# Kernel tuning notes

Hardware: AMD Instinct MI355X
Metric: run time of the kernel (lower is better)

The kernel has to match this reference:

```python
import jax, jax.numpy as jnp
import numpy as np

B, N, D = 4, 4096, 512
K = 16384          # codebook size
NUM_Q = 2          # residual quantizers (shared codebook)


def setup_inputs() -> dict:
    key = jax.random.key(0)
    ks = jax.random.split(key, 6)
    s = 1.0 / np.sqrt(D)
    return {
        "x": jax.random.normal(ks[0], (B, N, D), dtype=jnp.float32),
        "enc_w": jax.random.normal(ks[1], (D, D), dtype=jnp.float32) * s,
        "enc_b": jnp.zeros((D,), dtype=jnp.float32),
        "codebook": jax.random.normal(ks[2], (K, D), dtype=jnp.float32),
        "dec_w": jax.random.normal(ks[3], (D, D), dtype=jnp.float32) * s,
        "dec_b": jnp.zeros((D,), dtype=jnp.float32),
    }


def _residual_vq(z, codebook):
    # z: [B, N, D] -> flatten tokens
    flat = z.reshape(-1, z.shape[-1])          # [T, D]
    c_sq = jnp.sum(codebook * codebook, axis=-1)  # [K]
    q_sum = jnp.zeros_like(flat)
    residual = flat
    for _ in range(NUM_Q):
        # argmin of ||r - c||^2 == argmin of (||c||^2 - 2 r.c); skip ||r||^2
        dists = c_sq[None, :] - 2.0 * (residual @ codebook.T)  # [T, K]
        idx = jnp.argmin(dists, axis=-1)                       # [T]
        q = codebook[idx]                                      # gather [T, D]
        q_sum = q_sum + q
        residual = residual - q
    return q_sum.reshape(z.shape)


def reference(x, enc_w, enc_b, codebook, dec_w, dec_b):
    z = x @ enc_w.T + enc_b                     # encoder Linear(512 -> 512)
    q = _residual_vq(z, codebook)               # sum of per-stage code vectors
    z_tilde = z + jax.lax.stop_gradient(q - z)  # straight-through estimator
    x_recon = z_tilde @ dec_w.T + dec_b         # decoder Linear(512 -> 512)
    return x_recon
```

## Files before the change

### kernel.cpp

```cpp
#include <hip/hip_runtime.h>
#include <stdint.h>

constexpr int TT = 16384;
constexpr int DD = 512;
constexpr int KK = 16384;
constexpr int TOPK = 8;

typedef __bf16 bf16x8 __attribute__((ext_vector_type(8)));
typedef __bf16 bf16x4 __attribute__((ext_vector_type(4)));
typedef float f32x4 __attribute__((ext_vector_type(4)));

typedef const __attribute__((address_space(1))) void* gas_ptr;
typedef __attribute__((address_space(3))) void* las_ptr;

__device__ __forceinline__ unsigned long long pack_di(float d, int idx) {
    uint32_t u = __float_as_uint(d);
    u = (u & 0x80000000u) ? ~u : (u | 0x80000000u);
    return ((unsigned long long)u << 32) | (uint32_t)idx;
}

__device__ __forceinline__ unsigned long long umin64(unsigned long long a,
                                                     unsigned long long b) {
    return a < b ? a : b;
}

template<int MODE>
__global__ __launch_bounds__(256)
void gemm_mfma(const float* __restrict__ A, const float* __restrict__ A2,
               const float* __restrict__ W, const float* __restrict__ bias,
               float* __restrict__ out0, float* __restrict__ out1,
               __bf16* __restrict__ out2)
{
    __shared__ __bf16 Ah[128 * 64], Al[128 * 64];
    __shared__ __bf16 Bh[128 * 64], Bl[128 * 64];
    const int tid = threadIdx.x;
    const int lane = tid & 63;
    const int w = tid >> 6;
    const int row0 = blockIdx.y * 128;
    const int col0 = blockIdx.x * 128;

    f32x4 acc[2][8] = {};

    const int sr = tid >> 4;
    const int scol = (tid & 15) * 4;
    const int lcol = (((scol >> 3) ^ (sr & 7)) << 3) + (scol & 7);

    int a_off[2], b_off[8];
    #pragma unroll
    for (int mi = 0; mi < 2; ++mi) {
        const int ar = w * 32 + mi * 16 + (lane & 15);
        a_off[mi] = ar * 64 + (((lane >> 4) ^ (lane & 7)) << 3);
    }
    #pragma unroll
    for (int ni = 0; ni < 8; ++ni) {
        const int br = ni * 16 + (lane & 15);
        b_off[ni] = br * 64 + (((lane >> 4) ^ (lane & 7)) << 3);
    }

    for (int kb = 0; kb < 512; kb += 64) {
        __syncthreads();
        #pragma unroll
        for (int i = 0; i < 8; ++i) {
            const int r = i * 16 + sr;
            float4 v = *(const float4*)(A + (size_t)(row0 + r) * 512 + kb + scol);
            if (MODE == 1) {
                const float4 u = *(const float4*)(A2 + (size_t)(row0 + r) * 512 + kb + scol);
                v.x -= u.x; v.y -= u.y; v.z -= u.z; v.w -= u.w;
            }
            bf16x4 hv, lv;
            hv[0] = (__bf16)v.x; hv[1] = (__bf16)v.y; hv[2] = (__bf16)v.z; hv[3] = (__bf16)v.w;
            lv[0] = (__bf16)(v.x - (float)hv[0]); lv[1] = (__bf16)(v.y - (float)hv[1]);
            lv[2] = (__bf16)(v.z - (float)hv[2]); lv[3] = (__bf16)(v.w - (float)hv[3]);
            *(bf16x4*)(Ah + r * 64 + lcol) = hv;
            *(bf16x4*)(Al + r * 64 + lcol) = lv;

            const float4 x = *(const float4*)(W + (size_t)(col0 + r) * 512 + kb + scol);
            bf16x4 hw, lw;
            hw[0] = (__bf16)x.x; hw[1] = (__bf16)x.y; hw[2] = (__bf16)x.z; hw[3] = (__bf16)x.w;
            lw[0] = (__bf16)(x.x - (float)hw[0]); lw[1] = (__bf16)(x.y - (float)hw[1]);
            lw[2] = (__bf16)(x.z - (float)hw[2]); lw[3] = (__bf16)(x.w - (float)hw[3]);
            *(bf16x4*)(Bh + r * 64 + lcol) = hw;
            *(bf16x4*)(Bl + r * 64 + lcol) = lw;
        }
        __syncthreads();
        #pragma unroll
        for (int s = 0; s < 2; ++s) {
            const int sx = s * 32;
            bf16x8 ah[2], al[2];
            #pragma unroll
            for (int mi = 0; mi < 2; ++mi) {
                ah[mi] = *(const bf16x8*)(Ah + (a_off[mi] ^ sx));
                al[mi] = *(const bf16x8*)(Al + (a_off[mi] ^ sx));
            }
            #pragma unroll
            for (int ni = 0; ni < 8; ++ni) {
                const bf16x8 bh = *(const bf16x8*)(Bh + (b_off[ni] ^ sx));
                const bf16x8 bl = *(const bf16x8*)(Bl + (b_off[ni] ^ sx));
                #pragma unroll
                for (int mi = 0; mi < 2; ++mi) {
                    acc[mi][ni] = __builtin_amdgcn_mfma_f32_16x16x32_bf16(ah[mi], bh, acc[mi][ni], 0, 0, 0);
                    acc[mi][ni] = __builtin_amdgcn_mfma_f32_16x16x32_bf16(ah[mi], bl, acc[mi][ni], 0, 0, 0);
                    acc[mi][ni] = __builtin_amdgcn_mfma_f32_16x16x32_bf16(al[mi], bh, acc[mi][ni], 0, 0, 0);
                }
            }
        }
    }

    #pragma unroll
    for (int mi = 0; mi < 2; ++mi) {
        #pragma unroll
        for (int reg = 0; reg < 4; ++reg) {
            const int row = row0 + w * 32 + mi * 16 + (lane >> 4) * 4 + reg;
            #pragma unroll
            for (int ni = 0; ni < 8; ++ni) {
                const int col = col0 + ni * 16 + (lane & 15);
                const float o = acc[mi][ni][reg] + bias[col];
                out0[(size_t)row * 512 + col] = o;
                if (MODE == 0) {
                    out1[(size_t)row * 512 + col] = o;
                    out2[(size_t)row * 512 + col] = (__bf16)o;
                }
            }
        }
    }
}

__global__ __launch_bounds__(256)
void dist_approx(const __bf16* __restrict__ Rh,
                 const __bf16* __restrict__ Ch,
                 const float* __restrict__ csq,
                 unsigned long long* __restrict__ winners)
{
    __shared__ __bf16 As[128 * 64];
    __shared__ __bf16 Bs[128 * 64];
    const int tid = threadIdx.x;
    const int lane = tid & 63;
    const int w = tid >> 6;
    const int row0 = blockIdx.y * 128;
    const int col0 = blockIdx.x * 128;

    f32x4 acc[2][8] = {};

    const int gc = (lane & 7) ^ ((lane >> 3) & 7);
    const __bf16* Ab = Rh + (size_t)(row0 + w * 32 + (lane >> 3)) * 512 + gc * 8;
    const __bf16* Bb = Ch + (size_t)(col0 + w * 32 + (lane >> 3)) * 512 + gc * 8;
    __bf16* lA = As + (w * 32) * 64;
    __bf16* lB = Bs + (w * 32) * 64;

    int a_off[2], b_off[8];
    #pragma unroll
    for (int mi = 0; mi < 2; ++mi) {
        const int ar = w * 32 + mi * 16 + (lane & 15);
        a_off[mi] = ar * 64 + (((lane >> 4) ^ (lane & 7)) << 3);
    }
    #pragma unroll
    for (int ni = 0; ni < 8; ++ni) {
        const int br = ni * 16 + (lane & 15);
        b_off[ni] = br * 64 + (((lane >> 4) ^ (lane & 7)) << 3);
    }

    for (int kb = 0; kb < 512; kb += 64) {
        __syncthreads();
        #pragma unroll
        for (int j = 0; j < 4; ++j) {
            __builtin_amdgcn_global_load_lds(
                (gas_ptr)(Ab + (size_t)j * 8 * 512 + kb), (las_ptr)(lA + j * 8 * 64), 16, 0, 0);
            __builtin_amdgcn_global_load_lds(
                (gas_ptr)(Bb + (size_t)j * 8 * 512 + kb), (las_ptr)(lB + j * 8 * 64), 16, 0, 0);
        }
        __syncthreads();
        #pragma unroll
        for (int s = 0; s < 2; ++s) {
            const int sx = s * 32;
            bf16x8 af[2], bfr[8];
            #pragma unroll
            for (int mi = 0; mi < 2; ++mi) af[mi] = *(const bf16x8*)(As + (a_off[mi] ^ sx));
            #pragma unroll
            for (int ni = 0; ni < 8; ++ni) bfr[ni] = *(const bf16x8*)(Bs + (b_off[ni] ^ sx));
            #pragma unroll
            for (int mi = 0; mi < 2; ++mi)
                #pragma unroll
                for (int ni = 0; ni < 8; ++ni)
                    acc[mi][ni] = __builtin_amdgcn_mfma_f32_16x16x32_bf16(
                        af[mi], bfr[ni], acc[mi][ni], 0, 0, 0);
        }
    }

    float csv[8];
    #pragma unroll
    for (int ni = 0; ni < 8; ++ni)
        csv[ni] = csq[col0 + ni * 16 + (lane & 15)];

    #pragma unroll
    for (int mi = 0; mi < 2; ++mi) {
        #pragma unroll
        for (int reg = 0; reg < 4; ++reg) {
            unsigned long long b = ~0ull, s = ~0ull;
            #pragma unroll
            for (int ni = 0; ni < 8; ++ni) {
                const float d = fmaf(-2.0f, acc[mi][ni][reg], csv[ni]);
                const unsigned long long x = pack_di(d, col0 + ni * 16 + (lane & 15));
                const unsigned long long nb = umin64(b, x);
                s = umin64(s, b ^ x ^ nb);
                b = nb;
            }
            #pragma unroll
            for (int m = 1; m < 16; m <<= 1) {
                const unsigned long long ob = __shfl_xor(b, m, 16);
                const unsigned long long os = __shfl_xor(s, m, 16);
                const unsigned long long nb = umin64(b, ob);
                s = umin64(umin64(s, os), b ^ ob ^ nb);
                b = nb;
            }
            if ((lane & 15) == 0) {
                const int row = row0 + w * 32 + mi * 16 + (lane >> 4) * 4 + reg;
                winners[(size_t)row * 256 + blockIdx.x * 2 + 0] = b;
                winners[(size_t)row * 256 + blockIdx.x * 2 + 1] = s;
            }
        }
    }
}

__global__ __launch_bounds__(256)
void select_rescore(const unsigned long long* __restrict__ winners,
                    const float* __restrict__ CB, const float* __restrict__ csq,
                    float* __restrict__ R, __bf16* __restrict__ R16)
{
    const int w = threadIdx.x >> 6;
    const int lane = threadIdx.x & 63;
    const int token = blockIdx.x * 4 + w;

    const unsigned long long* wt = winners + (size_t)token * 256;
    unsigned long long v[4];
    #pragma unroll
    for (int j = 0; j < 4; ++j) v[j] = wt[lane * 4 + j];

    unsigned long long cand[TOPK];
    #pragma unroll
    for (int t = 0; t < TOPK; ++t) {
        unsigned long long mm = umin64(umin64(v[0], v[1]), umin64(v[2], v[3]));
        #pragma unroll
        for (int m = 1; m < 64; m <<= 1)
            mm = umin64(mm, __shfl_xor(mm, m, 64));
        cand[t] = mm;
        #pragma unroll
        for (int j = 0; j < 4; ++j) if (v[j] == mm) v[j] = ~0ull;
    }

    float4 r0 = *(const float4*)(R + (size_t)token * 512 + lane * 8);
    float4 r1 = *(const float4*)(R + (size_t)token * 512 + lane * 8 + 4);

    unsigned long long best = ~0ull;
    #pragma unroll
    for (int t = 0; t < TOPK; ++t) {
        const int col = (int)(cand[t] & 0xFFFFFFFFull);
        const float4 c0 = *(const float4*)(CB + (size_t)col * 512 + lane * 8);
        const float4 c1 = *(const float4*)(CB + (size_t)col * 512 + lane * 8 + 4);
        float dot = r0.x * c0.x;
        dot = fmaf(r0.y, c0.y, dot); dot = fmaf(r0.z, c0.z, dot);
        dot = fmaf(r0.w, c0.w, dot); dot = fmaf(r1.x, c1.x, dot);
        dot = fmaf(r1.y, c1.y, dot); dot = fmaf(r1.z, c1.z, dot);
        dot = fmaf(r1.w, c1.w, dot);
        #pragma unroll
        for (int m = 1; m < 64; m <<= 1) dot += __shfl_xor(dot, m, 64);
        const float d = fmaf(-2.0f, dot, csq[col]);
        best = umin64(best, pack_di(d, col));
    }

    const int bcol = (int)(best & 0xFFFFFFFFull);
    const float4 c0 = *(const float4*)(CB + (size_t)bcol * 512 + lane * 8);
    const float4 c1 = *(const float4*)(CB + (size_t)bcol * 512 + lane * 8 + 4);
    r0.x -= c0.x; r0.y -= c0.y; r0.z -= c0.z; r0.w -= c0.w;
    r1.x -= c1.x; r1.y -= c1.y; r1.z -= c1.z; r1.w -= c1.w;
    *(float4*)(R + (size_t)token * 512 + lane * 8) = r0;
    *(float4*)(R + (size_t)token * 512 + lane * 8 + 4) = r1;
    bf16x8 h;
    h[0] = (__bf16)r0.x; h[1] = (__bf16)r0.y; h[2] = (__bf16)r0.z; h[3] = (__bf16)r0.w;
    h[4] = (__bf16)r1.x; h[5] = (__bf16)r1.y; h[6] = (__bf16)r1.z; h[7] = (__bf16)r1.w;
    *(bf16x8*)(R16 + (size_t)token * 512 + lane * 8) = h;
}

__global__ __launch_bounds__(256)
void prep_cb(const float* __restrict__ CB, float* __restrict__ c_sq,
             __bf16* __restrict__ cb16)
{
    const int wave = threadIdx.x >> 6;
    const int lane = threadIdx.x & 63;
    const int row = blockIdx.x * 4 + wave;
    const float* p = CB + (size_t)row * DD + lane * 8;
    const float4 a = *(const float4*)p;
    const float4 b = *(const float4*)(p + 4);
    bf16x8 h;
    h[0] = (__bf16)a.x; h[1] = (__bf16)a.y; h[2] = (__bf16)a.z; h[3] = (__bf16)a.w;
    h[4] = (__bf16)b.x; h[5] = (__bf16)b.y; h[6] = (__bf16)b.z; h[7] = (__bf16)b.w;
    *(bf16x8*)(cb16 + (size_t)row * DD + lane * 8) = h;
    float s = a.x*a.x + a.y*a.y + a.z*a.z + a.w*a.w
            + b.x*b.x + b.y*b.y + b.z*b.z + b.w*b.w;
    #pragma unroll
    for (int m = 1; m < 64; m <<= 1) s += __shfl_xor(s, m, 64);
    if (lane == 0) c_sq[row] = s;
}

extern "C" void kernel_launch(void* const* d_in, const int* in_sizes, int n_in,
                              void* d_out, int out_size, void* d_ws, size_t ws_size,
                              hipStream_t stream)
{
    const float* x    = (const float*)d_in[0];
    const float* encw = (const float*)d_in[1];
    const float* encb = (const float*)d_in[2];
    const float* cb   = (const float*)d_in[3];
    const float* decw = (const float*)d_in[4];
    const float* decb = (const float*)d_in[5];
    float* out = (float*)d_out;

    float* z    = (float*)d_ws;
    float* r    = z + (size_t)TT * DD;
    __bf16* cb16 = (__bf16*)(r + (size_t)TT * DD);
    __bf16* r16  = cb16 + (size_t)KK * DD;
    float* csq  = (float*)(r16 + (size_t)TT * DD);
    unsigned long long* winners = (unsigned long long*)d_out;

    const dim3 blk(256);

    gemm_mfma<0><<<dim3(DD / 128, TT / 128), blk, 0, stream>>>(
        x, nullptr, encw, encb, z, r, r16);

    prep_cb<<<dim3(KK / 4), blk, 0, stream>>>(cb, csq, cb16);

    for (int s = 0; s < 2; ++s) {
        dist_approx<<<dim3(KK / 128, TT / 128), blk, 0, stream>>>(r16, cb16, csq, winners);
        select_rescore<<<dim3(TT / 4), blk, 0, stream>>>(winners, cb, csq, r, r16);
    }

    gemm_mfma<1><<<dim3(DD / 128, TT / 128), blk, 0, stream>>>(
        z, r, decw, decb, out, nullptr, nullptr);
}
```

Baseline: 1.126 ms.

## Enlarge distance GEMM tile to 128x256 with 2x2 warp layout, fix LDS swizzle

The distance kernel now computes a 128x256 output tile per block, with warps arranged 2x2 so each warp owns 64x128 and reuses A fragments across more MFMAs. That halves the A reload traffic per codebook column and raises MFMA work per LDS read, at the cost of doubling the accumulators and the B shared memory, which may reduce occupancy. Per-warp top-2 winners keep the same 128-column granularity, so the select kernel is unchanged. The LDS read swizzle now XORs with the row index instead of the lane index, matching the write-side pattern.

```diff
diff --git a/kernel.cpp b/kernel.cpp
--- a/kernel.cpp
+++ b/kernel.cpp
@@ -49,12 +49,12 @@
     #pragma unroll
     for (int mi = 0; mi < 2; ++mi) {
         const int ar = w * 32 + mi * 16 + (lane & 15);
-        a_off[mi] = ar * 64 + (((lane >> 4) ^ (lane & 7)) << 3);
+        a_off[mi] = ar * 64 + (((lane >> 4) ^ (ar & 7)) << 3);
     }
     #pragma unroll
     for (int ni = 0; ni < 8; ++ni) {
         const int br = ni * 16 + (lane & 15);
-        b_off[ni] = br * 64 + (((lane >> 4) ^ (lane & 7)) << 3);
+        b_off[ni] = br * 64 + (((lane >> 4) ^ (br & 7)) << 3);
     }
 
     for (int kb = 0; kb < 512; kb += 64) {
@@ -132,53 +132,55 @@
                  unsigned long long* __restrict__ winners)
 {
     __shared__ __bf16 As[128 * 64];
-    __shared__ __bf16 Bs[128 * 64];
+    __shared__ __bf16 Bs[256 * 64];
     const int tid = threadIdx.x;
     const int lane = tid & 63;
     const int w = tid >> 6;
+    const int wm = w >> 1, wn = w & 1;
     const int row0 = blockIdx.y * 128;
-    const int col0 = blockIdx.x * 128;
-
-    f32x4 acc[2][8] = {};
+    const int col0 = blockIdx.x * 256;
+
+    f32x4 acc[4][8] = {};
 
     const int gc = (lane & 7) ^ ((lane >> 3) & 7);
     const __bf16* Ab = Rh + (size_t)(row0 + w * 32 + (lane >> 3)) * 512 + gc * 8;
-    const __bf16* Bb = Ch + (size_t)(col0 + w * 32 + (lane >> 3)) * 512 + gc * 8;
+    const __bf16* Bb = Ch + (size_t)(col0 + w * 64 + (lane >> 3)) * 512 + gc * 8;
     __bf16* lA = As + (w * 32) * 64;
-    __bf16* lB = Bs + (w * 32) * 64;
-
-    int a_off[2], b_off[8];
-    #pragma unroll
-    for (int mi = 0; mi < 2; ++mi) {
-        const int ar = w * 32 + mi * 16 + (lane & 15);
-        a_off[mi] = ar * 64 + (((lane >> 4) ^ (lane & 7)) << 3);
+    __bf16* lB = Bs + (w * 64) * 64;
+
+    int a_off[4], b_off[8];
+    #pragma unroll
+    for (int mi = 0; mi < 4; ++mi) {
+        const int ar = wm * 64 + mi * 16 + (lane & 15);
+        a_off[mi] = ar * 64 + (((lane >> 4) ^ (ar & 7)) << 3);
     }
     #pragma unroll
     for (int ni = 0; ni < 8; ++ni) {
-        const int br = ni * 16 + (lane & 15);
-        b_off[ni] = br * 64 + (((lane >> 4) ^ (lane & 7)) << 3);
+        const int br = wn * 128 + ni * 16 + (lane & 15);
+        b_off[ni] = br * 64 + (((lane >> 4) ^ (br & 7)) << 3);
     }
 
     for (int kb = 0; kb < 512; kb += 64) {
         __syncthreads();
         #pragma unroll
-        for (int j = 0; j < 4; ++j) {
+        for (int j = 0; j < 4; ++j)
             __builtin_amdgcn_global_load_lds(
                 (gas_ptr)(Ab + (size_t)j * 8 * 512 + kb), (las_ptr)(lA + j * 8 * 64), 16, 0, 0);
+        #pragma unroll
+        for (int j = 0; j < 8; ++j)
             __builtin_amdgcn_global_load_lds(
                 (gas_ptr)(Bb + (size_t)j * 8 * 512 + kb), (las_ptr)(lB + j * 8 * 64), 16, 0, 0);
-        }
         __syncthreads();
         #pragma unroll
         for (int s = 0; s < 2; ++s) {
             const int sx = s * 32;
-            bf16x8 af[2], bfr[8];
-            #pragma unroll
-            for (int mi = 0; mi < 2; ++mi) af[mi] = *(const bf16x8*)(As + (a_off[mi] ^ sx));
+            bf16x8 af[4], bfr[8];
+            #pragma unroll
+            for (int mi = 0; mi < 4; ++mi) af[mi] = *(const bf16x8*)(As + (a_off[mi] ^ sx));
             #pragma unroll
             for (int ni = 0; ni < 8; ++ni) bfr[ni] = *(const bf16x8*)(Bs + (b_off[ni] ^ sx));
             #pragma unroll
-            for (int mi = 0; mi < 2; ++mi)
+            for (int mi = 0; mi < 4; ++mi)
                 #pragma unroll
                 for (int ni = 0; ni < 8; ++ni)
                     acc[mi][ni] = __builtin_amdgcn_mfma_f32_16x16x32_bf16(
@@ -189,17 +191,19 @@
     float csv[8];
     #pragma unroll
     for (int ni = 0; ni < 8; ++ni)
-        csv[ni] = csq[col0 + ni * 16 + (lane & 15)];
-
-    #pragma unroll
-    for (int mi = 0; mi < 2; ++mi) {
+        csv[ni] = csq[col0 + wn * 128 + ni * 16 + (lane & 15)];
+
+    const int tile = blockIdx.x * 2 + wn;
+    #pragma unroll
+    for (int mi = 0; mi < 4; ++mi) {
         #pragma unroll
         for (int reg = 0; reg < 4; ++reg) {
             unsigned long long b = ~0ull, s = ~0ull;
             #pragma unroll
             for (int ni = 0; ni < 8; ++ni) {
                 const float d = fmaf(-2.0f, acc[mi][ni][reg], csv[ni]);
-                const unsigned long long x = pack_di(d, col0 + ni * 16 + (lane & 15));
+                const unsigned long long x =
+                    pack_di(d, col0 + wn * 128 + ni * 16 + (lane & 15));
                 const unsigned long long nb = umin64(b, x);
                 s = umin64(s, b ^ x ^ nb);
                 b = nb;
@@ -213,9 +217,9 @@
                 b = nb;
             }
             if ((lane & 15) == 0) {
-                const int row = row0 + w * 32 + mi * 16 + (lane >> 4) * 4 + reg;
-                winners[(size_t)row * 256 + blockIdx.x * 2 + 0] = b;
-                winners[(size_t)row * 256 + blockIdx.x * 2 + 1] = s;
+                const int row = row0 + wm * 64 + mi * 16 + (lane >> 4) * 4 + reg;
+                winners[(size_t)row * 256 + tile * 2 + 0] = b;
+                winners[(size_t)row * 256 + tile * 2 + 1] = s;
             }
         }
     }
@@ -328,7 +332,7 @@
     prep_cb<<<dim3(KK / 4), blk, 0, stream>>>(cb, csq, cb16);
 
     for (int s = 0; s < 2; ++s) {
-        dist_approx<<<dim3(KK / 128, TT / 128), blk, 0, stream>>>(r16, cb16, csq, winners);
+        dist_approx<<<dim3(KK / 256, TT / 128), blk, 0, stream>>>(r16, cb16, csq, winners);
         select_rescore<<<dim3(TT / 4), blk, 0, stream>>>(winners, cb, csq, r, r16);
     }
 
```

Result: no change. 1.142 ms (+1.4%).
